# Kernel tuning notes

Measured on AMD Instinct MI355X. Metric: run time of the kernel, lower is better.

The kernel has to match this reference:

```python
import jax, jax.numpy as jnp
import numpy as np

D_MODEL = 1024
D_HEAD = 64

def setup_inputs() -> dict:
    key = jax.random.key(0)
    ks = jax.random.split(key, 7)
    s = 1.0 / np.sqrt(D_MODEL)
    x = jax.random.normal(ks[0], (4, 4096, D_MODEL), dtype=jnp.float32)
    Wq = jax.random.uniform(ks[1], (D_MODEL, D_HEAD), jnp.float32, -s, s)
    bq = jax.random.uniform(ks[2], (D_HEAD,), jnp.float32, -s, s)
    Wk = jax.random.uniform(ks[3], (D_MODEL, D_HEAD), jnp.float32, -s, s)
    bk = jax.random.uniform(ks[4], (D_HEAD,), jnp.float32, -s, s)
    Wv = jax.random.uniform(ks[5], (D_MODEL, D_HEAD), jnp.float32, -s, s)
    bv = jax.random.uniform(ks[6], (D_HEAD,), jnp.float32, -s, s)
    return {"x": x, "Wq": Wq, "bq": bq, "Wk": Wk, "bk": bk, "Wv": Wv, "bv": bv}

def reference(x, Wq, bq, Wk, bk, Wv, bv):
    # x: [b, s, d_model] -> Q,K,V: [b, s, d_head]
    Q = jnp.einsum('bsd,dh->bsh', x, Wq) + bq
    K = jnp.einsum('bsd,dh->bsh', x, Wk) + bk
    V = jnp.einsum('bsd,dh->bsh', x, Wv) + bv
    scale = 1.0 / jnp.sqrt(jnp.asarray(D_HEAD, x.dtype))
    scores = jnp.einsum('bqh,bkh->bqk', Q, K) * scale  # [b, s, s]
    attn = jax.nn.softmax(scores, axis=-1)
    return jnp.einsum('bqk,bkh->bqh', attn, V)  # [b, s, d_head]
```

## Files before the change

### kernel.cpp

```cpp
#include <hip/hip_runtime.h>

typedef __bf16 bf16x8 __attribute__((ext_vector_type(8)));
typedef __bf16 bf16x4 __attribute__((ext_vector_type(4)));
typedef float f32x4 __attribute__((ext_vector_type(4)));
typedef unsigned short u16x8 __attribute__((ext_vector_type(8)));

union FragU { u16x8 u; bf16x8 b; };
union PackU { bf16x4 v; unsigned long long q; };

__device__ __forceinline__ unsigned short bfbits(float f) {
  __bf16 h = (__bf16)f;
  union { __bf16 h; unsigned short s; } cv; cv.h = h;
  return cv.s;
}

#define MFMA16(a, b, c) __builtin_amdgcn_mfma_f32_16x16x32_bf16((a), (b), (c), 0, 0, 0)

#define QSCALE 0.18033688011112042f

__global__ __launch_bounds__(256) void wt_kernel(
    const float* __restrict__ Wq, const float* __restrict__ Wk, const float* __restrict__ Wv,
    unsigned short* __restrict__ WF)
{
  const int m = blockIdx.x >> 5;
  const int c = blockIdx.x & 31;
  const float* W = (m == 0) ? Wq : ((m == 1) ? Wk : Wv);
  const int t = threadIdx.x >> 6;
  const int lane = threadIdx.x & 63;
  const int l15 = lane & 15;
  const int g = lane >> 4;
  unsigned short* dst = WF + ((((size_t)m * 32 + c) * 4 + t) * 64 + lane) * 8;
#pragma unroll
  for (int e = 0; e < 8; ++e)
    dst[e] = bfbits(W[(size_t)(32 * c + 8 * g + e) * 64 + (16 * t + l15)]);
}

__global__ __launch_bounds__(256, 2) void proj_kernel(
    const float* __restrict__ x, const unsigned short* __restrict__ WF,
    const float* __restrict__ bq, const float* __restrict__ bk, const float* __restrict__ bv,
    unsigned short* __restrict__ Qb, unsigned short* __restrict__ KF,
    unsigned short* __restrict__ VF)
{
  __shared__ f32x4 part[2][2][3][4][64];
  const int tid = threadIdx.x;
  const int lane = tid & 63;
  const int wid = tid >> 6;
  const int rg = wid & 1;
  const int kh = wid >> 1;
  const int l15 = lane & 15;
  const int g = lane >> 4;
  const int row0 = blockIdx.x * 32 + rg * 16;

  f32x4 accQ[4], accK[4], accV[4];
  const f32x4 zero = {0.f, 0.f, 0.f, 0.f};
#pragma unroll
  for (int i = 0; i < 4; ++i) { accQ[i] = zero; accK[i] = zero; accV[i] = zero; }

  const float* xrow = x + (size_t)(row0 + l15) * 1024;

  f32x4 xx0[4], xx1[4];
  bf16x8 wq[2][4], wk[2][4], wv[2][4];

#define PLDX(XB, C) { xx0[XB] = *(const f32x4*)(xrow + 32 * (C) + 8 * g); \
                      xx1[XB] = *(const f32x4*)(xrow + 32 * (C) + 8 * g + 4); }
#define PLDW(WS, C) { _Pragma("unroll") for (int t = 0; t < 4; ++t) { \
    wq[WS][t] = *(const bf16x8*)(WF + ((((size_t)0 * 32 + (C)) * 4 + t) * 64 + lane) * 8); \
    wk[WS][t] = *(const bf16x8*)(WF + ((((size_t)1 * 32 + (C)) * 4 + t) * 64 + lane) * 8); \
    wv[WS][t] = *(const bf16x8*)(WF + ((((size_t)2 * 32 + (C)) * 4 + t) * 64 + lane) * 8); } }
#define PHALF(XB, WS, CXN, CWN) { \
    FragU xf; \
    _Pragma("unroll") for (int i = 0; i < 4; ++i) { \
      xf.b[i] = (__bf16)xx0[XB][i]; xf.b[4 + i] = (__bf16)xx1[XB][i]; } \
    if ((CXN) < cend) PLDX(XB, CXN); \
    _Pragma("unroll") for (int t = 0; t < 4; ++t) { \
      accQ[t] = MFMA16(xf.b, wq[WS][t], accQ[t]); \
      accK[t] = MFMA16(xf.b, wk[WS][t], accK[t]); \
      accV[t] = MFMA16(wv[WS][t], xf.b, accV[t]); } \
    if ((CWN) < cend) PLDW(WS, CWN); }

  const int c0 = kh * 16;
  const int cend = c0 + 16;
  PLDX(0, c0) PLDX(1, c0 + 1) PLDX(2, c0 + 2) PLDX(3, c0 + 3)
  PLDW(0, c0) PLDW(1, c0 + 1)

#pragma unroll 1
  for (int c = c0; c < cend; c += 4) {
    PHALF(0, 0, c + 4, c + 2)
    PHALF(1, 1, c + 5, c + 3)
    PHALF(2, 0, c + 6, c + 4)
    PHALF(3, 1, c + 7, c + 5)
  }

#pragma unroll
  for (int t = 0; t < 4; ++t) {
    part[kh][rg][0][t][lane] = accQ[t];
    part[kh][rg][1][t][lane] = accK[t];
    part[kh][rg][2][t][lane] = accV[t];
  }
  __syncthreads();

  const int erg = wid & 1;
  const int b = blockIdx.x >> 7;
  const int q0 = (blockIdx.x * 32 + erg * 16) & 4095;
  const int kt = q0 >> 6;
  const int r16 = (q0 >> 4) & 3;
  f32x4 s[4];
  if (wid < 2) {
#pragma unroll
    for (int t = 0; t < 4; ++t) {
      const f32x4 p0 = part[0][erg][0][t][lane];
      const f32x4 p1 = part[1][erg][0][t][lane];
#pragma unroll
      for (int i = 0; i < 4; ++i) s[t][i] = p0[i] + p1[i];
    }
    unsigned short* Qbase = Qb + (size_t)b * 4096 * 64;
#pragma unroll
    for (int t = 0; t < 4; ++t) {
      const float bqv = bq[16 * t + l15];
#pragma unroll
      for (int r = 0; r < 4; ++r)
        Qbase[(size_t)(q0 + 4 * g + r) * 64 + 16 * t + l15] =
            bfbits((s[t][r] + bqv) * QSCALE);
    }
#pragma unroll
    for (int t = 0; t < 4; ++t) {
      const f32x4 p0 = part[0][erg][2][t][lane];
      const f32x4 p1 = part[1][erg][2][t][lane];
#pragma unroll
      for (int i = 0; i < 4; ++i) s[t][i] = p0[i] + p1[i];
    }
    unsigned short* VFb = VF + ((size_t)b * 64 + kt) * 4096;
#pragma unroll
    for (int t = 0; t < 4; ++t) {
#pragma unroll
      for (int r = 0; r < 4; ++r) {
        const int hv = 16 * t + 4 * g + r;
        VFb[(size_t)((t * 2 + (r16 >> 1)) * 64 + (r16 & 1) * 32 + (l15 >> 3) * 16 + 4 * g + r) * 8 +
            (l15 & 7)] = bfbits(s[t][r] + bv[hv]);
      }
    }
  } else {
#pragma unroll
    for (int t = 0; t < 4; ++t) {
      const f32x4 p0 = part[0][erg][1][t][lane];
      const f32x4 p1 = part[1][erg][1][t][lane];
#pragma unroll
      for (int i = 0; i < 4; ++i) s[t][i] = p0[i] + p1[i];
    }
    unsigned short* KFb = KF + ((size_t)b * 64 + kt) * 4096;
#pragma unroll
    for (int t = 0; t < 4; ++t) {
      const float bkv = bk[16 * t + l15];
#pragma unroll
      for (int r = 0; r < 4; ++r)
        KFb[(size_t)((r16 * 2 + (t >> 1)) * 64 + (t & 1) * 32 + (l15 >> 3) * 16 + 4 * g + r) * 8 +
            (l15 & 7)] = bfbits(s[t][r] + bkv);
    }
  }
}

__global__ __launch_bounds__(256, 2) void flash_kernel(
    const unsigned short* __restrict__ Qb, const unsigned short* __restrict__ KF,
    const unsigned short* __restrict__ VF, float* __restrict__ out)
{
  __shared__ __align__(16) unsigned char lds[36864];
  const int tid = threadIdx.x;
  const int lane = tid & 63;
  const int w = tid >> 6;
  const int l15 = lane & 15;
  const int g = lane >> 4;
  const int bid = blockIdx.x;
  const int xcd = bid & 7;
  const int b = xcd >> 1;
  const int qt = (bid >> 3) * 2 + (xcd & 1);
  const int q0 = qt * 32;

  const unsigned short* Qp = Qb + (size_t)b * 4096 * 64;
  const unsigned short* KFb = KF + (size_t)b * 262144;
  const unsigned short* VFb = VF + (size_t)b * 262144;

  const bf16x8 qfA0 = *(const bf16x8*)(Qp + (size_t)(q0 + l15) * 64 + 8 * g);
  const bf16x8 qfA1 = *(const bf16x8*)(Qp + (size_t)(q0 + l15) * 64 + 32 + 8 * g);
  const bf16x8 qfB0 = *(const bf16x8*)(Qp + (size_t)(q0 + 16 + l15) * 64 + 8 * g);
  const bf16x8 qfB1 = *(const bf16x8*)(Qp + (size_t)(q0 + 16 + l15) * 64 + 32 + 8 * g);

  f32x4 O_A[4], O_B[4];
  const f32x4 zero = {0.f, 0.f, 0.f, 0.f};
#pragma unroll
  for (int i = 0; i < 4; ++i) { O_A[i] = zero; O_B[i] = zero; }
  float mA = -INFINITY, lA = 0.f, mB = -INFINITY, lB = 0.f;
  unsigned short* PwA = (unsigned short*)lds + (w * 2 + 0) * 1152;
  unsigned short* PwB = (unsigned short*)lds + (w * 2 + 1) * 1152;

#define SM_HALF(S, mvar, lvar, OA, PW) { \
  float mt = fmaxf(fmaxf(S[0][0], S[0][1]), fmaxf(S[0][2], S[0][3])); \
  _Pragma("unroll") for (int t = 1; t < 4; ++t) \
    _Pragma("unroll") for (int r = 0; r < 4; ++r) mt = fmaxf(mt, S[t][r]); \
  mt = fmaxf(mt, __shfl_xor(mt, 16)); \
  mt = fmaxf(mt, __shfl_xor(mt, 32)); \
  if (!__all(mt <= mvar + 8.0f)) { \
    const float mnew = fmaxf(mvar, mt); \
    const float alpha = __builtin_amdgcn_exp2f(mvar - mnew); \
    mvar = mnew; lvar *= alpha; \
    _Pragma("unroll") for (int r = 0; r < 4; ++r) { \
      const float ar = __shfl(alpha, 4 * g + r); \
      OA[0][r] *= ar; OA[1][r] *= ar; OA[2][r] *= ar; OA[3][r] *= ar; } \
  } \
  float ps = 0.f; \
  _Pragma("unroll") for (int t = 0; t < 4; ++t) { \
    const float p0 = __builtin_amdgcn_exp2f(S[t][0] - mvar); \
    const float p1 = __builtin_amdgcn_exp2f(S[t][1] - mvar); \
    const float p2 = __builtin_amdgcn_exp2f(S[t][2] - mvar); \
    const float p3 = __builtin_amdgcn_exp2f(S[t][3] - mvar); \
    ps += (p0 + p1) + (p2 + p3); \
    PackU pk_; pk_.v[0] = (__bf16)p0; pk_.v[1] = (__bf16)p1; \
    pk_.v[2] = (__bf16)p2; pk_.v[3] = (__bf16)p3; \
    *(unsigned long long*)((PW) + l15 * 72 + 16 * t + 4 * g) = pk_.q; } \
  ps += __shfl_xor(ps, 16); \
  ps += __shfl_xor(ps, 32); \
  lvar += ps; }

#pragma unroll 1
  for (int kt = w; kt < 64; kt += 4) {
    const unsigned short* Kt = KFb + kt * 4096;
    const unsigned short* Vt = VFb + kt * 4096;
    bf16x8 kf[8], vf[8];
#pragma unroll
    for (int j = 0; j < 8; ++j) kf[j] = *(const bf16x8*)(Kt + (j * 64 + lane) * 8);
#pragma unroll
    for (int j = 0; j < 8; ++j) vf[j] = *(const bf16x8*)(Vt + (j * 64 + lane) * 8);
    f32x4 S_A[4], S_B[4];
#pragma unroll
    for (int t = 0; t < 4; ++t) {
      S_A[t] = zero;
      S_A[t] = MFMA16(kf[2 * t], qfA0, S_A[t]);
      S_A[t] = MFMA16(kf[2 * t + 1], qfA1, S_A[t]);
      S_B[t] = zero;
      S_B[t] = MFMA16(kf[2 * t], qfB0, S_B[t]);
      S_B[t] = MFMA16(kf[2 * t + 1], qfB1, S_B[t]);
    }
    SM_HALF(S_A, mA, lA, O_A, PwA)
    SM_HALF(S_B, mB, lB, O_B, PwB)
#pragma unroll
    for (int s = 0; s < 2; ++s) {
      const bf16x8 paA = *(const bf16x8*)(PwA + l15 * 72 + 32 * s + 8 * g);
      const bf16x8 paB = *(const bf16x8*)(PwB + l15 * 72 + 32 * s + 8 * g);
#pragma unroll
      for (int nt = 0; nt < 4; ++nt) {
        O_A[nt] = MFMA16(paA, vf[2 * nt + s], O_A[nt]);
        O_B[nt] = MFMA16(paB, vf[2 * nt + s], O_B[nt]);
      }
    }
  }

  __syncthreads();
  float* O_l = (float*)lds;
  float* mlp = (float*)(lds + 34816);
#pragma unroll
  for (int nt = 0; nt < 4; ++nt)
#pragma unroll
    for (int r = 0; r < 4; ++r) {
      O_l[((w * 2 + 0) * 16 + 4 * g + r) * 68 + 16 * nt + l15] = O_A[nt][r];
      O_l[((w * 2 + 1) * 16 + 4 * g + r) * 68 + 16 * nt + l15] = O_B[nt][r];
    }
  if (g == 0) {
    mlp[((w * 2 + 0) * 16 + l15) * 2] = mA; mlp[((w * 2 + 0) * 16 + l15) * 2 + 1] = lA;
    mlp[((w * 2 + 1) * 16 + l15) * 2] = mB; mlp[((w * 2 + 1) * 16 + l15) * 2 + 1] = lB;
  }
  __syncthreads();

  const int q = tid >> 3;
  const int h0 = (tid & 7) * 8;
  const int qh = q >> 4, qr = q & 15;
  float M = -INFINITY;
#pragma unroll
  for (int s = 0; s < 4; ++s) M = fmaxf(M, mlp[((s * 2 + qh) * 16 + qr) * 2]);
  float L = 0.f;
  f32x4 a0 = zero, a1 = zero;
#pragma unroll
  for (int s = 0; s < 4; ++s) {
    const int rowi = (s * 2 + qh) * 16 + qr;
    const float wgt = __builtin_amdgcn_exp2f(mlp[rowi * 2] - M);
    L += wgt * mlp[rowi * 2 + 1];
    const f32x4 o0 = *(const f32x4*)&O_l[rowi * 68 + h0];
    const f32x4 o1 = *(const f32x4*)&O_l[rowi * 68 + h0 + 4];
#pragma unroll
    for (int i = 0; i < 4; ++i) { a0[i] += wgt * o0[i]; a1[i] += wgt * o1[i]; }
  }
  const float inv = 1.0f / L;
  float* ob = out + ((size_t)b * 4096 + qt * 32 + q) * 64 + h0;
  f32x4 r0 = {a0[0] * inv, a0[1] * inv, a0[2] * inv, a0[3] * inv};
  f32x4 r1 = {a1[0] * inv, a1[1] * inv, a1[2] * inv, a1[3] * inv};
  *(f32x4*)ob = r0;
  *(f32x4*)(ob + 4) = r1;
}

extern "C" void kernel_launch(void* const* d_in, const int* in_sizes, int n_in,
                              void* d_out, int out_size, void* d_ws, size_t ws_size,
                              hipStream_t stream) {
  const float* x  = (const float*)d_in[0];
  const float* Wq = (const float*)d_in[1];
  const float* bq = (const float*)d_in[2];
  const float* Wk = (const float*)d_in[3];
  const float* bk = (const float*)d_in[4];
  const float* Wv = (const float*)d_in[5];
  const float* bv = (const float*)d_in[6];

  char* ws = (char*)d_ws;
  unsigned short* WF = (unsigned short*)ws;
  unsigned short* Qb = (unsigned short*)(ws + (512u << 10));
  unsigned short* KF = (unsigned short*)(ws + (512u << 10) + (2u << 20));
  unsigned short* VF = (unsigned short*)(ws + (512u << 10) + (4u << 20));
  float* out = (float*)d_out;

  hipLaunchKernelGGL(wt_kernel,    dim3(96),  dim3(256), 0, stream, Wq, Wk, Wv, WF);
  hipLaunchKernelGGL(proj_kernel,  dim3(512), dim3(256), 0, stream, x, WF, bq, bk, bv, Qb, KF, VF);
  hipLaunchKernelGGL(flash_kernel, dim3(512), dim3(256), 0, stream, Qb, KF, VF, out);
}
```

Baseline: 62.00 us.

## Stage projection weights through LDS via async global_load_lds pipeline and set MFMA priority

The projection kernel stops loading weight fragments into registers per wave. Instead the two row-group waves cooperatively DMA each K-chunk's weights into a triple-buffered LDS ring with global_load_lds, using explicit vmcnt waits and barriers in a fully unrolled 16-step pipeline. This removes the duplicate global weight loads across row groups and frees the registers the weights occupied, at the cost of a barrier per step and LDS reads. Separately, the flash kernel raises wave priority around its MFMA blocks with s_setprio so matrix work is favoured over softmax in other waves.

```diff
diff --git a/kernel.cpp b/kernel.cpp
--- a/kernel.cpp
+++ b/kernel.cpp
@@ -41,7 +41,7 @@
     unsigned short* __restrict__ Qb, unsigned short* __restrict__ KF,
     unsigned short* __restrict__ VF)
 {
-  __shared__ f32x4 part[2][2][3][4][64];
+  __shared__ __align__(16) unsigned short ldsW[2][3][6144];
   const int tid = threadIdx.x;
   const int lane = tid & 63;
   const int wid = tid >> 6;
@@ -50,6 +50,7 @@
   const int l15 = lane & 15;
   const int g = lane >> 4;
   const int row0 = blockIdx.x * 32 + rg * 16;
+  const int c0 = kh * 16;
 
   f32x4 accQ[4], accK[4], accV[4];
   const f32x4 zero = {0.f, 0.f, 0.f, 0.f};
@@ -57,45 +58,68 @@
   for (int i = 0; i < 4; ++i) { accQ[i] = zero; accK[i] = zero; accV[i] = zero; }
 
   const float* xrow = x + (size_t)(row0 + l15) * 1024;
-
   f32x4 xx0[4], xx1[4];
-  bf16x8 wq[2][4], wk[2][4], wv[2][4];
+
+#define WDMA(CC) { const int sl_ = (CC) % 3; \
+    _Pragma("unroll") for (int j_ = 0; j_ < 6; ++j_) { \
+      const int f_ = rg * 6 + j_; \
+      const int m_ = f_ >> 2, t_ = f_ & 3; \
+      const unsigned short* gs_ = WF + ((((size_t)m_ * 32 + (CC)) * 4 + t_) * 64 + lane) * 8; \
+      __builtin_amdgcn_global_load_lds( \
+          (const __attribute__((address_space(1))) void*)gs_, \
+          (__attribute__((address_space(3))) void*)&ldsW[kh][sl_][f_ * 512], \
+          16, 0, 0); } }
 
 #define PLDX(XB, C) { xx0[XB] = *(const f32x4*)(xrow + 32 * (C) + 8 * g); \
                       xx1[XB] = *(const f32x4*)(xrow + 32 * (C) + 8 * g + 4); }
-#define PLDW(WS, C) { _Pragma("unroll") for (int t = 0; t < 4; ++t) { \
-    wq[WS][t] = *(const bf16x8*)(WF + ((((size_t)0 * 32 + (C)) * 4 + t) * 64 + lane) * 8); \
-    wk[WS][t] = *(const bf16x8*)(WF + ((((size_t)1 * 32 + (C)) * 4 + t) * 64 + lane) * 8); \
-    wv[WS][t] = *(const bf16x8*)(WF + ((((size_t)2 * 32 + (C)) * 4 + t) * 64 + lane) * 8); } }
-#define PHALF(XB, WS, CXN, CWN) { \
+
+#define SUBIT(CC, KK, WIMM, DOW, DOX) { \
+    asm volatile("s_waitcnt vmcnt(" #WIMM ")" ::: "memory"); \
+    __builtin_amdgcn_s_barrier(); \
+    __builtin_amdgcn_sched_barrier(0); \
+    if (DOW) WDMA((CC) + 2); \
     FragU xf; \
-    _Pragma("unroll") for (int i = 0; i < 4; ++i) { \
-      xf.b[i] = (__bf16)xx0[XB][i]; xf.b[4 + i] = (__bf16)xx1[XB][i]; } \
-    if ((CXN) < cend) PLDX(XB, CXN); \
-    _Pragma("unroll") for (int t = 0; t < 4; ++t) { \
-      accQ[t] = MFMA16(xf.b, wq[WS][t], accQ[t]); \
-      accK[t] = MFMA16(xf.b, wk[WS][t], accK[t]); \
-      accV[t] = MFMA16(wv[WS][t], xf.b, accV[t]); } \
-    if ((CWN) < cend) PLDW(WS, CWN); }
-
-  const int c0 = kh * 16;
-  const int cend = c0 + 16;
-  PLDX(0, c0) PLDX(1, c0 + 1) PLDX(2, c0 + 2) PLDX(3, c0 + 3)
-  PLDW(0, c0) PLDW(1, c0 + 1)
-
-#pragma unroll 1
-  for (int c = c0; c < cend; c += 4) {
-    PHALF(0, 0, c + 4, c + 2)
-    PHALF(1, 1, c + 5, c + 3)
-    PHALF(2, 0, c + 6, c + 4)
-    PHALF(3, 1, c + 7, c + 5)
-  }
-
+    _Pragma("unroll") for (int i_ = 0; i_ < 4; ++i_) { \
+      xf.b[i_] = (__bf16)xx0[KK][i_]; xf.b[4 + i_] = (__bf16)xx1[KK][i_]; } \
+    if (DOX) PLDX(KK, (CC) + 4); \
+    { const int rs_ = (CC) % 3; \
+      _Pragma("unroll") for (int t = 0; t < 4; ++t) { \
+        const bf16x8 wq_ = *(const bf16x8*)&ldsW[kh][rs_][(0 * 4 + t) * 512 + lane * 8]; \
+        const bf16x8 wk_ = *(const bf16x8*)&ldsW[kh][rs_][(1 * 4 + t) * 512 + lane * 8]; \
+        const bf16x8 wv_ = *(const bf16x8*)&ldsW[kh][rs_][(2 * 4 + t) * 512 + lane * 8]; \
+        accQ[t] = MFMA16(xf.b, wq_, accQ[t]); \
+        accK[t] = MFMA16(xf.b, wk_, accK[t]); \
+        accV[t] = MFMA16(wv_, xf.b, accV[t]); } } }
+
+  PLDX(0, c0 + 0) PLDX(1, c0 + 1) PLDX(2, c0 + 2) PLDX(3, c0 + 3)
+  WDMA(c0)
+  __builtin_amdgcn_sched_barrier(0);
+  WDMA(c0 + 1)
+
+  SUBIT(c0 + 0,  0, 6,  1, 1)
+  SUBIT(c0 + 1,  1, 8,  1, 1)
+  SUBIT(c0 + 2,  2, 10, 1, 1)
+  SUBIT(c0 + 3,  3, 10, 1, 1)
+  SUBIT(c0 + 4,  0, 10, 1, 1)
+  SUBIT(c0 + 5,  1, 10, 1, 1)
+  SUBIT(c0 + 6,  2, 10, 1, 1)
+  SUBIT(c0 + 7,  3, 10, 1, 1)
+  SUBIT(c0 + 8,  0, 10, 1, 1)
+  SUBIT(c0 + 9,  1, 10, 1, 1)
+  SUBIT(c0 + 10, 2, 10, 1, 1)
+  SUBIT(c0 + 11, 3, 10, 1, 1)
+  SUBIT(c0 + 12, 0, 10, 1, 0)
+  SUBIT(c0 + 13, 1, 8,  1, 0)
+  SUBIT(c0 + 14, 2, 6,  0, 0)
+  SUBIT(c0 + 15, 3, 0,  0, 0)
+
+  __syncthreads();
+  f32x4* part = (f32x4*)ldsW;
 #pragma unroll
   for (int t = 0; t < 4; ++t) {
-    part[kh][rg][0][t][lane] = accQ[t];
-    part[kh][rg][1][t][lane] = accK[t];
-    part[kh][rg][2][t][lane] = accV[t];
+    part[(size_t)((kh * 2 + rg) * 12 + 0 * 4 + t) * 64 + lane] = accQ[t];
+    part[(size_t)((kh * 2 + rg) * 12 + 1 * 4 + t) * 64 + lane] = accK[t];
+    part[(size_t)((kh * 2 + rg) * 12 + 2 * 4 + t) * 64 + lane] = accV[t];
   }
   __syncthreads();
 
@@ -108,8 +132,8 @@
   if (wid < 2) {
 #pragma unroll
     for (int t = 0; t < 4; ++t) {
-      const f32x4 p0 = part[0][erg][0][t][lane];
-      const f32x4 p1 = part[1][erg][0][t][lane];
+      const f32x4 p0 = part[(size_t)((0 * 2 + erg) * 12 + 0 * 4 + t) * 64 + lane];
+      const f32x4 p1 = part[(size_t)((1 * 2 + erg) * 12 + 0 * 4 + t) * 64 + lane];
 #pragma unroll
       for (int i = 0; i < 4; ++i) s[t][i] = p0[i] + p1[i];
     }
@@ -124,8 +148,8 @@
     }
 #pragma unroll
     for (int t = 0; t < 4; ++t) {
-      const f32x4 p0 = part[0][erg][2][t][lane];
-      const f32x4 p1 = part[1][erg][2][t][lane];
+      const f32x4 p0 = part[(size_t)((0 * 2 + erg) * 12 + 2 * 4 + t) * 64 + lane];
+      const f32x4 p1 = part[(size_t)((1 * 2 + erg) * 12 + 2 * 4 + t) * 64 + lane];
 #pragma unroll
       for (int i = 0; i < 4; ++i) s[t][i] = p0[i] + p1[i];
     }
@@ -142,8 +166,8 @@
   } else {
 #pragma unroll
     for (int t = 0; t < 4; ++t) {
-      const f32x4 p0 = part[0][erg][1][t][lane];
-      const f32x4 p1 = part[1][erg][1][t][lane];
+      const f32x4 p0 = part[(size_t)((0 * 2 + erg) * 12 + 1 * 4 + t) * 64 + lane];
+      const f32x4 p1 = part[(size_t)((1 * 2 + erg) * 12 + 1 * 4 + t) * 64 + lane];
 #pragma unroll
       for (int i = 0; i < 4; ++i) s[t][i] = p0[i] + p1[i];
     }
@@ -230,6 +254,7 @@
 #pragma unroll
     for (int j = 0; j < 8; ++j) vf[j] = *(const bf16x8*)(Vt + (j * 64 + lane) * 8);
     f32x4 S_A[4], S_B[4];
+    __builtin_amdgcn_s_setprio(1);
 #pragma unroll
     for (int t = 0; t < 4; ++t) {
       S_A[t] = zero;
@@ -239,8 +264,10 @@
       S_B[t] = MFMA16(kf[2 * t], qfB0, S_B[t]);
       S_B[t] = MFMA16(kf[2 * t + 1], qfB1, S_B[t]);
     }
+    __builtin_amdgcn_s_setprio(0);
     SM_HALF(S_A, mA, lA, O_A, PwA)
     SM_HALF(S_B, mB, lB, O_B, PwB)
+    __builtin_amdgcn_s_setprio(1);
 #pragma unroll
     for (int s = 0; s < 2; ++s) {
       const bf16x8 paA = *(const bf16x8*)(PwA + l15 * 72 + 32 * s + 8 * g);
@@ -251,6 +278,7 @@
         O_B[nt] = MFMA16(paB, vf[2 * nt + s], O_B[nt]);
       }
     }
+    __builtin_amdgcn_s_setprio(0);
   }
 
   __syncthreads();
```

New measurement: 58.25 us. 1.06x faster.
